# Kernel tuning notes

Measured on AMD Instinct MI355X. Metric: run time of the kernel, lower is better.

The kernel has to match this reference:

```python
import jax, jax.numpy as jnp
import numpy as np

EPS = 1e-6
NQ, NKV, D, HID = 40, 8, 128, 5120
QKV_DIM = (NQ + 2 * NKV) * D + NQ  # gating enabled


def rmsnorm(x, w):
    xf = x.astype(jnp.float32)
    n = jax.lax.rsqrt(jnp.mean(xf * xf, axis=-1, keepdims=True) + EPS)
    return (xf * n).astype(x.dtype) * w


def rope(x, cos, sin):
    # x: [B,S,h,d], cos/sin: [B,S,d]
    d = x.shape[-1]
    c = cos[..., None, :d]
    s = sin[..., None, :d]
    x1, x2 = x[..., : d // 2], x[..., d // 2 :]
    rot = jnp.concatenate([-x2, x1], axis=-1)
    return x * c + rot * s


def setup_inputs() -> dict:
    key = jax.random.key(0)
    ks = jax.random.split(key, 8)
    B, S = 1, 2048
    return {
        "x": jax.random.normal(ks[0], (B, S, HID), jnp.float32),
        "rope_cos": jax.random.normal(ks[1], (B, S, D), jnp.float32),
        "rope_sin": jax.random.normal(ks[2], (B, S, D), jnp.float32),
        "w_pre_norm": jnp.ones((HID,), jnp.float32),
        "w_qkv": jax.random.normal(ks[3], (HID, QKV_DIM), jnp.float32) * 0.02,
        "w_q_norm": jnp.ones((D,), jnp.float32),
        "w_k_norm": jnp.ones((D,), jnp.float32),
        "w_proj": jax.random.normal(ks[4], (NQ * D, HID), jnp.float32) * 0.02,
    }


def reference(x, rope_cos, rope_sin, w_pre_norm, w_qkv, w_q_norm, w_k_norm, w_proj):
    B, S, _ = x.shape
    normed = rmsnorm(x, w_pre_norm)
    qkv = normed @ w_qkv  # [B,S,QKV_DIM]
    q_dim, k_dim = NQ * D, NKV * D
    q = qkv[..., :q_dim].reshape(B, S, NQ, D)
    k = qkv[..., q_dim : q_dim + k_dim].reshape(B, S, NKV, D)
    v = qkv[..., q_dim + k_dim : q_dim + 2 * k_dim].reshape(B, S, NKV, D)
    gate = jax.nn.sigmoid(qkv[..., q_dim + 2 * k_dim :])  # [B,S,NQ]
    q = rmsnorm(q, w_q_norm)
    k = rmsnorm(k, w_k_norm)
    q = rope(q, rope_cos, rope_sin)
    k = rope(k, rope_cos, rope_sin)
    # GQA: expand kv groups to query heads
    rep = NQ // NKV
    k = jnp.repeat(k, rep, axis=2)  # [B,S,NQ,D]
    v = jnp.repeat(v, rep, axis=2)
    scale = 1.0 / jnp.sqrt(jnp.float32(D))
    scores = jnp.einsum("bqhd,bkhd->bhqk", q, k) * scale
    attn = jax.nn.softmax(scores, axis=-1)
    out = jnp.einsum("bhqk,bkhd->bqhd", attn, v)  # [B,S,NQ,D]
    out = out * gate[..., None]
    out = out.reshape(B, S, NQ * D)
    return out @ w_proj
```

## Files before the change

### kernel.cpp

```cpp
#include <hip/hip_runtime.h>
#include <hip/hip_bf16.h>
#include <stdint.h>

#define S_LEN 2048
#define NQh   40
#define NKVh  8
#define HD    128
#define HIDd  5120
#define QKV_C 7208
#define QKV_P 7424
#define NROW  (S_LEN * NQh)

typedef unsigned short u16;
typedef short bf16x8 __attribute__((ext_vector_type(8)));
typedef float f32x4  __attribute__((ext_vector_type(4)));
typedef u16   u16x4  __attribute__((ext_vector_type(4)));

typedef const __attribute__((address_space(1))) void* gas_ptr;
typedef __attribute__((address_space(3))) void*       las_ptr;

#define MFMA16(a, b, c) __builtin_amdgcn_mfma_f32_16x16x32_bf16(a, b, c, 0, 0, 0)

__device__ __forceinline__ u16 f2bf(float f) {
  union { float f; unsigned u; } v; v.f = f;
  return (u16)((v.u + 0x7fffu + ((v.u >> 16) & 1u)) >> 16);
}
__device__ __forceinline__ u16 f2bf_c(float f) {
  union { __hip_bfloat16 b; u16 u; } v;
  v.b = __float2bfloat16(f);
  return v.u;
}
__device__ __forceinline__ float b2f(u16 b) {
  union { unsigned u; float f; } v; v.u = ((unsigned)b) << 16; return v.f;
}

__device__ __forceinline__ float wave_sum64(float x) {
#pragma unroll
  for (int m = 32; m > 0; m >>= 1) x += __shfl_xor(x, m, 64);
  return x;
}

__global__ __launch_bounds__(256) void prenorm_kernel(
    const float* __restrict__ x, const float* __restrict__ w, u16* __restrict__ xn) {
  int row = blockIdx.x;
  const float4* xr = (const float4*)(x + (size_t)row * HIDd);
  const float4* wr = (const float4*)w;
  float4 vx[5];
  float ss = 0.f;
#pragma unroll
  for (int c = 0; c < 5; ++c) {
    int i = c * 256 + threadIdx.x;
    vx[c] = xr[i];
    ss += vx[c].x * vx[c].x + vx[c].y * vx[c].y + vx[c].z * vx[c].z + vx[c].w * vx[c].w;
  }
  ss = wave_sum64(ss);
  __shared__ float red[4];
  if ((threadIdx.x & 63) == 0) red[threadIdx.x >> 6] = ss;
  __syncthreads();
  float tot = red[0] + red[1] + red[2] + red[3];
  float n = rsqrtf(tot * (1.f / HIDd) + 1e-6f);
  u16x4* out = (u16x4*)(xn + (size_t)row * HIDd);
#pragma unroll
  for (int c = 0; c < 5; ++c) {
    int i = c * 256 + threadIdx.x;
    float4 vw = wr[i];
    u16x4 o;
    o.x = f2bf(vx[c].x * n * vw.x);
    o.y = f2bf(vx[c].y * n * vw.y);
    o.z = f2bf(vx[c].z * n * vw.z);
    o.w = f2bf(vx[c].w * n * vw.w);
    out[i] = o;
  }
}

__global__ __launch_bounds__(256) void transpose_cvt(
    const float* __restrict__ src, u16* __restrict__ dst,
    int C, long ld_src, long ld_dst, long srcZ, long dstZ) {
  src += (long)blockIdx.z * srcZ;
  dst += (long)blockIdx.z * dstZ;
  __shared__ float t[32][34];
  int c0 = blockIdx.x * 32, r0 = blockIdx.y * 32;
  {
    int lc = threadIdx.x & 15, lr = threadIdx.x >> 4;
#pragma unroll
    for (int i = 0; i < 32; i += 16) {
      int r = r0 + lr + i;
      int c = c0 + lc * 2;
      float2 v = make_float2(0.f, 0.f);
      if (c < C) v = *(const float2*)(src + (long)r * ld_src + c);
      *(float2*)&t[lr + i][lc * 2] = v;
    }
  }
  __syncthreads();
  {
    int cc = threadIdx.x >> 3;
    int rq = (threadIdx.x & 7) * 4;
    int c = c0 + cc;
    if (c < C) {
      u16x4 o;
#pragma unroll
      for (int rr = 0; rr < 4; ++rr) o[rr] = f2bf(t[rq + rr][cc]);
      *(u16x4*)(dst + (long)c * ld_dst + (r0 + rq)) = o;
    }
  }
}

__global__ __launch_bounds__(512, 1) void gemm8(
    const u16* __restrict__ A, const u16* __restrict__ BT, float* __restrict__ C,
    int M, int N, int K) {
  __shared__ __align__(16) char AL[65536];
  __shared__ __align__(16) char BL[65536];

  int tid = threadIdx.x, w = tid >> 6, l = tid & 63;
  int wm = w >> 2, wn = w & 3;
  int g = l >> 4, q = l & 15;

  int nwg = gridDim.x * gridDim.y;
  int wgid = blockIdx.y * gridDim.x + blockIdx.x;
  int cpx = nwg >> 3;
  int swz = (wgid & 7) * cpx + (wgid >> 3);
  int bx = swz % gridDim.x, by = swz / gridDim.x;
  long mBase = (long)by * 256, nBase = (long)bx * 256;
  long Kb = (long)K * 2;
  const char* Ag = (const char*)A + mBase * Kb;
  const char* Bg = (const char*)BT + nBase * Kb;

  int d0 = tid * 16, d1 = 8192 + tid * 16;
  long soff0 = (long)(d0 >> 6) * Kb + ((d0 & 63) ^ (((d0 >> 7) & 3) << 4));
  long soff1 = (long)(d1 >> 6) * Kb + ((d1 & 63) ^ (((d1 >> 7) & 3) << 4));

#define STG1(GBASE, LDSB, BUF, KH, T_)                                          \
  do {                                                                          \
    long kb_ = (long)(T_) * 128 + (KH) * 64;                                    \
    __builtin_amdgcn_global_load_lds((gas_ptr)((GBASE) + soff0 + kb_),          \
        (las_ptr)((LDSB) + (BUF) * 32768 + (KH) * 16384 + d0), 16, 0, 0);       \
    __builtin_amdgcn_global_load_lds((gas_ptr)((GBASE) + soff1 + kb_),          \
        (las_ptr)((LDSB) + (BUF) * 32768 + (KH) * 16384 + d1), 16, 0, 0);       \
  } while (0)

#define BARR                                                                    \
  do {                                                                          \
    __builtin_amdgcn_s_barrier();                                               \
    __builtin_amdgcn_sched_barrier(0);                                          \
  } while (0)
#define VMW(NLIT)                                                               \
  do {                                                                          \
    asm volatile("s_waitcnt vmcnt(" #NLIT ")" ::: "memory");                    \
    __builtin_amdgcn_sched_barrier(0);                                          \
  } while (0)

  int offA[8], offB[4];
#pragma unroll
  for (int i = 0; i < 8; ++i) {
    int r = wm * 128 + i * 16 + q;
    offA[i] = r * 64 + ((g * 16) ^ (((r >> 1) & 3) << 4));
  }
#pragma unroll
  for (int j = 0; j < 4; ++j) {
    int r = wn * 64 + j * 16 + q;
    offB[j] = r * 64 + ((g * 16) ^ (((r >> 1) & 3) << 4));
  }

#define RD_ALL(ABASE, BBASE)                                                    \
  do {                                                                          \
    _Pragma("unroll") for (int ii = 0; ii < 8; ++ii)                            \
      af[ii] = *(const bf16x8*)((ABASE) + offA[ii]);                            \
    _Pragma("unroll") for (int j = 0; j < 4; ++j)                               \
      bfr[j] = *(const bf16x8*)((BBASE) + offB[j]);                             \
  } while (0)
#define MFMA32                                                                  \
  do {                                                                          \
    __builtin_amdgcn_s_setprio(1);                                              \
    _Pragma("unroll") for (int ii = 0; ii < 8; ++ii)                            \
      _Pragma("unroll") for (int j = 0; j < 4; ++j)                             \
        acc[ii][j] = MFMA16(af[ii], bfr[j], acc[ii][j]);                        \
    __builtin_amdgcn_s_setprio(0);                                              \
  } while (0)

  f32x4 acc[8][4] = {};
  int NT = K >> 6;

  STG1(Ag, AL, 0, 0, 0); STG1(Bg, BL, 0, 0, 0);
  STG1(Ag, AL, 0, 1, 0); STG1(Bg, BL, 0, 1, 0);
  STG1(Ag, AL, 1, 0, 1); STG1(Bg, BL, 1, 0, 1);
  VMW(8); BARR;

  for (int t = 0; t < NT; ++t) {
    int buf = t & 1, nb = buf ^ 1;
    const char* Abuf = AL + buf * 32768;
    const char* Bbuf = BL + buf * 32768;
    bf16x8 af[8], bfr[4];

    RD_ALL(Abuf, Bbuf);
    if (t + 1 < NT) { STG1(Ag, AL, nb, 1, t + 1); STG1(Bg, BL, nb, 1, t + 1); VMW(8); }
    else            { VMW(0); }
    BARR;
    MFMA32;
    BARR;

    RD_ALL(Abuf + 16384, Bbuf + 16384);
    if (t + 2 < NT)      { STG1(Ag, AL, buf, 0, t + 2); STG1(Bg, BL, buf, 0, t + 2); VMW(8); }
    else if (t + 1 < NT) { VMW(4); }
    BARR;
    MFMA32;
    BARR;
  }
#undef STG1
#undef RD_ALL
#undef MFMA32
#undef BARR
#undef VMW

#pragma unroll
  for (int i = 0; i < 8; ++i)
#pragma unroll
    for (int j = 0; j < 4; ++j) {
      long mrow = mBase + wm * 128 + i * 16 + g * 4;
      long ncol = nBase + wn * 64 + j * 16 + q;
      float* cp = C + mrow * N + ncol;
#pragma unroll
      for (int r = 0; r < 4; ++r) cp[(long)r * N] = acc[i][j][r];
    }
}

__global__ __launch_bounds__(256) void split_kernel(
    const float* __restrict__ qkv, const float* __restrict__ cosb,
    const float* __restrict__ sinb, const float* __restrict__ wq,
    const float* __restrict__ wk, u16* __restrict__ qb, u16* __restrict__ kb,
    float* __restrict__ gate) {
  int s = blockIdx.x;
  int w = threadIdx.x >> 6, l = threadIdx.x & 63;
  const float* row = qkv + (size_t)s * QKV_P;
  float c0 = cosb[s * HD + l],      s0 = sinb[s * HD + l];
  float c1 = cosb[s * HD + 64 + l], s1 = sinb[s * HD + 64 + l];
  const float SCALE = 0.12751743f;
  for (int h = w; h < NQh; h += 4) {
    float x0 = row[h * HD + l], x1 = row[h * HD + 64 + l];
    float ss = wave_sum64(x0 * x0 + x1 * x1);
    float n = rsqrtf(ss * (1.f / HD) + 1e-6f);
    x0 *= n * wq[l]; x1 *= n * wq[64 + l];
    qb[((size_t)s * NQh + h) * HD + l]      = f2bf((x0 * c0 - x1 * s0) * SCALE);
    qb[((size_t)s * NQh + h) * HD + 64 + l] = f2bf((x1 * c1 + x0 * s1) * SCALE);
  }
  for (int h = w; h < NKVh; h += 4) {
    float x0 = row[NQh * HD + h * HD + l], x1 = row[NQh * HD + h * HD + 64 + l];
    float ss = wave_sum64(x0 * x0 + x1 * x1);
    float n = rsqrtf(ss * (1.f / HD) + 1e-6f);
    x0 *= n * wk[l]; x1 *= n * wk[64 + l];
    kb[((size_t)h * S_LEN + s) * HD + l]      = f2bf(x0 * c0 - x1 * s0);
    kb[((size_t)h * S_LEN + s) * HD + 64 + l] = f2bf(x1 * c1 + x0 * s1);
  }
  if (threadIdx.x < NQh) {
    float gx = row[(NQh + 2 * NKVh) * HD + threadIdx.x];
    gate[(size_t)s * NQh + threadIdx.x] = 1.f / (1.f + expf(-gx));
  }
}

__global__ __launch_bounds__(256) void attn_kernel(
    const u16* __restrict__ qb, const u16* __restrict__ kb,
    const u16* __restrict__ vT,
    u16* __restrict__ opart, float* __restrict__ lpart) {
  int L = blockIdx.x;
  int xcd = L & 7, t0 = L >> 3;
  int G = xcd * 10 + (t0 >> 4);
  int bx = t0 & 15;
  int h = G % NQh, z = G / NQh;
  int hk = h / 5;
  int w = threadIdx.x >> 6, l = threadIdx.x & 63;
  int g = l >> 4, q = l & 15;
  int s0 = bx * 128 + w * 32;
  int tid = threadIdx.x;

  __shared__ __align__(16) u16 Ks[2][32 * 128];
  __shared__ __align__(16) u16 Vs[2][128 * 32];
  __shared__ __align__(16) u16 Plds[4][2][16][40];

  bf16x8 ones;
#pragma unroll
  for (int j = 0; j < 8; ++j) ones[j] = (short)0x3F80;

  bf16x8 qf[2][4];
#pragma unroll
  for (int p = 0; p < 2; ++p)
#pragma unroll
    for (int kk = 0; kk < 4; ++kk)
      qf[p][kk] = *(const bf16x8*)(qb + ((size_t)(s0 + p * 16 + q) * NQh + h) * HD + kk * 32 + g * 8);

  const char* KhB = (const char*)(kb + ((size_t)hk * S_LEN + z * 1024) * HD);
  const char* VhB = (const char*)(vT + (size_t)hk * HD * S_LEN + z * 1024);

  int Dk0 = tid * 16, Dk1 = 4096 + tid * 16;
  long ks0 = (long)(Dk0 >> 8) * 256 + ((Dk0 & 255) ^ (((Dk0 >> 8) & 7) << 4));
  long ks1 = (long)(Dk1 >> 8) * 256 + ((Dk1 & 255) ^ (((Dk1 >> 8) & 7) << 4));
  long vs0 = (long)(Dk0 >> 6) * 4096 + ((Dk0 & 63) ^ (((Dk0 >> 7) & 3) << 4));
  long vs1 = (long)(Dk1 >> 6) * 4096 + ((Dk1 & 63) ^ (((Dk1 >> 7) & 3) << 4));

#define STG(BUF, T_)                                                            \
  do {                                                                          \
    __builtin_amdgcn_global_load_lds((gas_ptr)(KhB + (long)(T_) * 8192 + ks0),  \
        (las_ptr)((char*)&Ks[BUF][0] + Dk0), 16, 0, 0);                         \
    __builtin_amdgcn_global_load_lds((gas_ptr)(KhB + (long)(T_) * 8192 + ks1),  \
        (las_ptr)((char*)&Ks[BUF][0] + Dk1), 16, 0, 0);                         \
    __builtin_amdgcn_global_load_lds((gas_ptr)(VhB + (long)(T_) * 64 + vs0),    \
        (las_ptr)((char*)&Vs[BUF][0] + Dk0), 16, 0, 0);                         \
    __builtin_amdgcn_global_load_lds((gas_ptr)(VhB + (long)(T_) * 64 + vs1),    \
        (las_ptr)((char*)&Vs[BUF][0] + Dk1), 16, 0, 0);                         \
  } while (0)

#define BARR                                                                    \
  do {                                                                          \
    __builtin_amdgcn_sched_barrier(0);                                          \
    __builtin_amdgcn_s_barrier();                                               \
    __builtin_amdgcn_sched_barrier(0);                                          \
  } while (0)

  f32x4 oacc[8][2] = {};
  f32x4 lacc[2] = {};
  int xq = (q & 7) << 4;
  int xv = ((q >> 1) & 3) << 4;

  STG(0, 0); STG(1, 1);
  __builtin_amdgcn_sched_barrier(0);
  asm volatile("s_waitcnt vmcnt(4)" ::: "memory");
  BARR;

  for (int step = 0; step < 32; ++step) {
    const char* kc = (const char*)&Ks[step & 1][0];
    const char* vc = (const char*)&Vs[step & 1][0];

    f32x4 sacc[2][2] = {};
#pragma unroll
    for (int kk = 0; kk < 4; ++kk) {
#pragma unroll
      for (int kt = 0; kt < 2; ++kt) {
        bf16x8 kf = *(const bf16x8*)(kc + (kt * 16 + q) * 256 + ((kk * 64 + g * 16) ^ xq));
        sacc[kt][0] = MFMA16(kf, qf[0][kk], sacc[kt][0]);
        sacc[kt][1] = MFMA16(kf, qf[1][kk], sacc[kt][1]);
      }
    }
    bf16x8 va[8];
#pragma unroll
    for (int dt = 0; dt < 8; ++dt)
      va[dt] = *(const bf16x8*)(vc + (dt * 16 + q) * 64 + ((g * 16) ^ xv));

#pragma unroll
    for (int p = 0; p < 2; ++p) {
#pragma unroll
      for (int kt = 0; kt < 2; ++kt) {
        u16x4 pk;
#pragma unroll
        for (int r = 0; r < 4; ++r) pk[r] = f2bf_c(exp2f(sacc[kt][p][r]));
        *(u16x4*)&Plds[w][p][q][kt * 16 + g * 4] = pk;
      }
    }
    bf16x8 pf0 = *(const bf16x8*)&Plds[w][0][q][g * 8];
    bf16x8 pf1 = *(const bf16x8*)&Plds[w][1][q][g * 8];
    __builtin_amdgcn_s_setprio(1);
#pragma unroll
    for (int dt = 0; dt < 8; ++dt) {
      oacc[dt][0] = MFMA16(va[dt], pf0, oacc[dt][0]);
      oacc[dt][1] = MFMA16(va[dt], pf1, oacc[dt][1]);
    }
    lacc[0] = MFMA16(ones, pf0, lacc[0]);
    lacc[1] = MFMA16(ones, pf1, lacc[1]);
    __builtin_amdgcn_s_setprio(0);

    BARR;
    if (step + 2 < 32) {
      STG(step & 1, step + 2);
      __builtin_amdgcn_sched_barrier(0);
      asm volatile("s_waitcnt vmcnt(4)" ::: "memory");
      __builtin_amdgcn_sched_barrier(0);
    } else if (step + 1 < 32) {
      __builtin_amdgcn_sched_barrier(0);
      asm volatile("s_waitcnt vmcnt(0)" ::: "memory");
      __builtin_amdgcn_sched_barrier(0);
    }
    BARR;
  }
#undef STG
#undef BARR

#pragma unroll
  for (int p = 0; p < 2; ++p) {
    size_t row = (size_t)(s0 + p * 16 + q) * NQh + h;
    if (g == 0) lpart[(size_t)z * NROW + row] = lacc[p][0];
    u16* op = opart + ((size_t)z * NROW + row) * HD;
#pragma unroll
    for (int dt = 0; dt < 8; ++dt) {
      u16x4 o;
#pragma unroll
      for (int r = 0; r < 4; ++r) o[r] = f2bf_c(oacc[dt][p][r]);
      *(u16x4*)(op + dt * 16 + g * 4) = o;
    }
  }
}

__global__ __launch_bounds__(256) void combine_kernel(
    const u16* __restrict__ opart, const float* __restrict__ lpart,
    const float* __restrict__ gate, u16* __restrict__ ob) {
  int t = blockIdx.x * 256 + threadIdx.x;
  int row = t >> 5, dv = (t & 31) * 4;
  float l0 = lpart[row], l1 = lpart[NROW + row];
  float sc = gate[row] / (l0 + l1);
  u16x4 o0 = *(const u16x4*)(opart + (size_t)row * HD + dv);
  u16x4 o1 = *(const u16x4*)(opart + (size_t)NROW * HD + (size_t)row * HD + dv);
  u16x4 o;
#pragma unroll
  for (int r = 0; r < 4; ++r) o[r] = f2bf(sc * (b2f(o0[r]) + b2f(o1[r])));
  *(u16x4*)(ob + (size_t)row * HD + dv) = o;
}

extern "C" void kernel_launch(void* const* d_in, const int* in_sizes, int n_in,
                              void* d_out, int out_size, void* d_ws, size_t ws_size,
                              hipStream_t stream) {
  const float* x     = (const float*)d_in[0];
  const float* rc    = (const float*)d_in[1];
  const float* rs    = (const float*)d_in[2];
  const float* wpre  = (const float*)d_in[3];
  const float* wqkv  = (const float*)d_in[4];
  const float* wqn   = (const float*)d_in[5];
  const float* wkn   = (const float*)d_in[6];
  const float* wproj = (const float*)d_in[7];
  float* out = (float*)d_out;

  char* ws = (char*)d_ws;
  size_t off = 0;
  auto alloc = [&](size_t bytes) -> void* {
    void* p = ws + off;
    off += (bytes + 255) & ~(size_t)255;
    return p;
  };
  u16*   xn     = (u16*)  alloc((size_t)S_LEN * HIDd * 2);
  u16*   wqkvT  = (u16*)  alloc((size_t)QKV_P * HIDd * 2);
  u16*   wprojT = (u16*)  alloc((size_t)HIDd * HIDd * 2);
  float* qkv    = (float*)alloc((size_t)S_LEN * QKV_P * 4);
  u16*   qb     = (u16*)  alloc((size_t)S_LEN * NQh * HD * 2);
  u16*   kb     = (u16*)  alloc((size_t)NKVh * S_LEN * HD * 2);
  u16*   vT     = (u16*)  alloc((size_t)NKVh * HD * S_LEN * 2);
  float* gate   = (float*)alloc((size_t)S_LEN * NQh * 4);
  u16*   ob     = (u16*)  alloc((size_t)S_LEN * NQh * HD * 2);
  if (off > ws_size) return;

  u16*   opart = (u16*)ws;
  float* lpart = (float*)(opart + (size_t)2 * NROW * HD);

  prenorm_kernel<<<S_LEN, 256, 0, stream>>>(x, wpre, xn);
  transpose_cvt<<<dim3(QKV_P / 32, HIDd / 32, 1), 256, 0, stream>>>(
      wqkv, wqkvT, QKV_C, (long)QKV_C, (long)HIDd, 0, 0);
  transpose_cvt<<<dim3(HIDd / 32, HIDd / 32, 1), 256, 0, stream>>>(
      wproj, wprojT, HIDd, (long)HIDd, (long)HIDd, 0, 0);
  gemm8<<<dim3(QKV_P / 256, S_LEN / 256), 512, 0, stream>>>(
      xn, wqkvT, qkv, S_LEN, QKV_P, HIDd);
  split_kernel<<<S_LEN, 256, 0, stream>>>(qkv, rc, rs, wqn, wkn, qb, kb, gate);
  transpose_cvt<<<dim3(HD / 32, S_LEN / 32, NKVh), 256, 0, stream>>>(
      qkv + (NQh + NKVh) * HD, vT, HD, (long)QKV_P, (long)S_LEN,
      128, (long)HD * S_LEN);
  attn_kernel<<<1280, 256, 0, stream>>>(qb, kb, vT, opart, lpart);
  combine_kernel<<<NROW * 32 / 256, 256, 0, stream>>>(
      opart, lpart, gate, ob);
  gemm8<<<dim3(HIDd / 256, S_LEN / 256), 512, 0, stream>>>(
      ob, wprojT, out, S_LEN, HIDd, HIDd);
}
```

Baseline: 622.7 us.

## Store QKV GEMM output as bf16 and use 256x128 tiles for output projection

The QKV projection GEMM now writes bf16 instead of fp32. This halves its write traffic and the reads in split_kernel, and the V transpose becomes a plain bf16 transpose. The gemm8 kernel is templated on N-tile width and output type, and the output projection uses BN=128, which doubles its workgroup count from 160 to 320 so the GPU's compute units are better filled. The cost is extra rounding of Q/K/V/gate to bf16 before normalization, and lower B reuse per tile in the projection.

```diff
diff --git a/kernel.cpp b/kernel.cpp
--- a/kernel.cpp
+++ b/kernel.cpp
@@ -38,6 +38,15 @@
 #pragma unroll
   for (int m = 32; m > 0; m >>= 1) x += __shfl_xor(x, m, 64);
   return x;
+}
+
+__device__ __forceinline__ void cstore(float* cp, long strideN, const f32x4& v) {
+#pragma unroll
+  for (int r = 0; r < 4; ++r) cp[(long)r * strideN] = v[r];
+}
+__device__ __forceinline__ void cstore(u16* cp, long strideN, const f32x4& v) {
+#pragma unroll
+  for (int r = 0; r < 4; ++r) cp[(long)r * strideN] = f2bf_c(v[r]);
 }
 
 __global__ __launch_bounds__(256) void prenorm_kernel(
@@ -105,11 +114,39 @@
   }
 }
 
+__global__ __launch_bounds__(256) void transpose_bf16(
+    const u16* __restrict__ src, u16* __restrict__ dst,
+    long ld_src, long ld_dst, long srcZ, long dstZ) {
+  src += (long)blockIdx.z * srcZ;
+  dst += (long)blockIdx.z * dstZ;
+  __shared__ u16 t[32][34];
+  int c0 = blockIdx.x * 32, r0 = blockIdx.y * 32;
+  {
+    int lc = threadIdx.x & 15, lr = threadIdx.x >> 4;
+#pragma unroll
+    for (int i = 0; i < 32; i += 16)
+      *(unsigned*)&t[lr + i][lc * 2] =
+          *(const unsigned*)(src + (long)(r0 + lr + i) * ld_src + c0 + lc * 2);
+  }
+  __syncthreads();
+  {
+    int cc = threadIdx.x >> 3;
+    int rq = (threadIdx.x & 7) * 4;
+    u16x4 o;
+#pragma unroll
+    for (int rr = 0; rr < 4; ++rr) o[rr] = t[rq + rr][cc];
+    *(u16x4*)(dst + (long)(c0 + cc) * ld_dst + (r0 + rq)) = o;
+  }
+}
+
+template<int BN, typename OutT>
 __global__ __launch_bounds__(512, 1) void gemm8(
-    const u16* __restrict__ A, const u16* __restrict__ BT, float* __restrict__ C,
+    const u16* __restrict__ A, const u16* __restrict__ BT, OutT* __restrict__ C,
     int M, int N, int K) {
+  constexpr int NJ = BN / 64;
+  constexpr int BHALF = BN * 64;
   __shared__ __align__(16) char AL[65536];
-  __shared__ __align__(16) char BL[65536];
+  __shared__ __align__(16) char BL[4 * BHALF];
 
   int tid = threadIdx.x, w = tid >> 6, l = tid & 63;
   int wm = w >> 2, wn = w & 3;
@@ -120,7 +157,7 @@
   int cpx = nwg >> 3;
   int swz = (wgid & 7) * cpx + (wgid >> 3);
   int bx = swz % gridDim.x, by = swz / gridDim.x;
-  long mBase = (long)by * 256, nBase = (long)bx * 256;
+  long mBase = (long)by * 256, nBase = (long)bx * BN;
   long Kb = (long)K * 2;
   const char* Ag = (const char*)A + mBase * Kb;
   const char* Bg = (const char*)BT + nBase * Kb;
@@ -129,13 +166,22 @@
   long soff0 = (long)(d0 >> 6) * Kb + ((d0 & 63) ^ (((d0 >> 7) & 3) << 4));
   long soff1 = (long)(d1 >> 6) * Kb + ((d1 & 63) ^ (((d1 >> 7) & 3) << 4));
 
-#define STG1(GBASE, LDSB, BUF, KH, T_)                                          \
+#define STGA(BUF, KH, T_)                                                       \
   do {                                                                          \
     long kb_ = (long)(T_) * 128 + (KH) * 64;                                    \
-    __builtin_amdgcn_global_load_lds((gas_ptr)((GBASE) + soff0 + kb_),          \
-        (las_ptr)((LDSB) + (BUF) * 32768 + (KH) * 16384 + d0), 16, 0, 0);       \
-    __builtin_amdgcn_global_load_lds((gas_ptr)((GBASE) + soff1 + kb_),          \
-        (las_ptr)((LDSB) + (BUF) * 32768 + (KH) * 16384 + d1), 16, 0, 0);       \
+    __builtin_amdgcn_global_load_lds((gas_ptr)(Ag + soff0 + kb_),               \
+        (las_ptr)(AL + (BUF) * 32768 + (KH) * 16384 + d0), 16, 0, 0);           \
+    __builtin_amdgcn_global_load_lds((gas_ptr)(Ag + soff1 + kb_),               \
+        (las_ptr)(AL + (BUF) * 32768 + (KH) * 16384 + d1), 16, 0, 0);           \
+  } while (0)
+#define STGB(BUF, KH, T_)                                                       \
+  do {                                                                          \
+    long kb_ = (long)(T_) * 128 + (KH) * 64;                                    \
+    __builtin_amdgcn_global_load_lds((gas_ptr)(Bg + soff0 + kb_),               \
+        (las_ptr)(BL + (BUF) * 2 * BHALF + (KH) * BHALF + d0), 16, 0, 0);       \
+    if constexpr (BN == 256)                                                    \
+      __builtin_amdgcn_global_load_lds((gas_ptr)(Bg + soff1 + kb_),             \
+          (las_ptr)(BL + (BUF) * 2 * BHALF + (KH) * BHALF + d1), 16, 0, 0);     \
   } while (0)
 
 #define BARR                                                                    \
@@ -143,21 +189,33 @@
     __builtin_amdgcn_s_barrier();                                               \
     __builtin_amdgcn_sched_barrier(0);                                          \
   } while (0)
-#define VMW(NLIT)                                                               \
-  do {                                                                          \
-    asm volatile("s_waitcnt vmcnt(" #NLIT ")" ::: "memory");                    \
+#define VMW2                                                                    \
+  do {                                                                          \
+    if constexpr (BN == 256) asm volatile("s_waitcnt vmcnt(8)" ::: "memory");   \
+    else                     asm volatile("s_waitcnt vmcnt(6)" ::: "memory");   \
     __builtin_amdgcn_sched_barrier(0);                                          \
   } while (0)
-
-  int offA[8], offB[4];
+#define VMW1                                                                    \
+  do {                                                                          \
+    if constexpr (BN == 256) asm volatile("s_waitcnt vmcnt(4)" ::: "memory");   \
+    else                     asm volatile("s_waitcnt vmcnt(3)" ::: "memory");   \
+    __builtin_amdgcn_sched_barrier(0);                                          \
+  } while (0)
+#define VMW0                                                                    \
+  do {                                                                          \
+    asm volatile("s_waitcnt vmcnt(0)" ::: "memory");                            \
+    __builtin_amdgcn_sched_barrier(0);                                          \
+  } while (0)
+
+  int offA[8], offB[NJ];
 #pragma unroll
   for (int i = 0; i < 8; ++i) {
     int r = wm * 128 + i * 16 + q;
     offA[i] = r * 64 + ((g * 16) ^ (((r >> 1) & 3) << 4));
   }
 #pragma unroll
-  for (int j = 0; j < 4; ++j) {
-    int r = wn * 64 + j * 16 + q;
+  for (int j = 0; j < NJ; ++j) {
+    int r = wn * (BN / 4) + j * 16 + q;
     offB[j] = r * 64 + ((g * 16) ^ (((r >> 1) & 3) << 4));
   }
 
@@ -165,77 +223,78 @@
   do {                                                                          \
     _Pragma("unroll") for (int ii = 0; ii < 8; ++ii)                            \
       af[ii] = *(const bf16x8*)((ABASE) + offA[ii]);                            \
-    _Pragma("unroll") for (int j = 0; j < 4; ++j)                               \
+    _Pragma("unroll") for (int j = 0; j < NJ; ++j)                              \
       bfr[j] = *(const bf16x8*)((BBASE) + offB[j]);                             \
   } while (0)
-#define MFMA32                                                                  \
+#define MFMA_ALL                                                                \
   do {                                                                          \
     __builtin_amdgcn_s_setprio(1);                                              \
     _Pragma("unroll") for (int ii = 0; ii < 8; ++ii)                            \
-      _Pragma("unroll") for (int j = 0; j < 4; ++j)                             \
+      _Pragma("unroll") for (int j = 0; j < NJ; ++j)                            \
         acc[ii][j] = MFMA16(af[ii], bfr[j], acc[ii][j]);                        \
     __builtin_amdgcn_s_setprio(0);                                              \
   } while (0)
 
-  f32x4 acc[8][4] = {};
+  f32x4 acc[8][NJ] = {};
   int NT = K >> 6;
 
-  STG1(Ag, AL, 0, 0, 0); STG1(Bg, BL, 0, 0, 0);
-  STG1(Ag, AL, 0, 1, 0); STG1(Bg, BL, 0, 1, 0);
-  STG1(Ag, AL, 1, 0, 1); STG1(Bg, BL, 1, 0, 1);
-  VMW(8); BARR;
+  STGA(0, 0, 0); STGB(0, 0, 0);
+  STGA(0, 1, 0); STGB(0, 1, 0);
+  STGA(1, 0, 1); STGB(1, 0, 1);
+  VMW2; BARR;
 
   for (int t = 0; t < NT; ++t) {
     int buf = t & 1, nb = buf ^ 1;
     const char* Abuf = AL + buf * 32768;
-    const char* Bbuf = BL + buf * 32768;
-    bf16x8 af[8], bfr[4];
+    const char* Bbuf = BL + buf * 2 * BHALF;
+    bf16x8 af[8], bfr[NJ];
 
     RD_ALL(Abuf, Bbuf);
-    if (t + 1 < NT) { STG1(Ag, AL, nb, 1, t + 1); STG1(Bg, BL, nb, 1, t + 1); VMW(8); }
-    else            { VMW(0); }
+    if (t + 1 < NT) { STGA(nb, 1, t + 1); STGB(nb, 1, t + 1); VMW2; }
+    else            { VMW0; }
     BARR;
-    MFMA32;
+    MFMA_ALL;
     BARR;
 
-    RD_ALL(Abuf + 16384, Bbuf + 16384);
-    if (t + 2 < NT)      { STG1(Ag, AL, buf, 0, t + 2); STG1(Bg, BL, buf, 0, t + 2); VMW(8); }
-    else if (t + 1 < NT) { VMW(4); }
+    RD_ALL(Abuf + 16384, Bbuf + BHALF);
+    if (t + 2 < NT)      { STGA(buf, 0, t + 2); STGB(buf, 0, t + 2); VMW2; }
+    else if (t + 1 < NT) { VMW1; }
     BARR;
-    MFMA32;
+    MFMA_ALL;
     BARR;
   }
-#undef STG1
+#undef STGA
+#undef STGB
 #undef RD_ALL
-#undef MFMA32
+#undef MFMA_ALL
 #undef BARR
-#undef VMW
+#undef VMW2
+#undef VMW1
+#undef VMW0
 
 #pragma unroll
   for (int i = 0; i < 8; ++i)
 #pragma unroll
-    for (int j = 0; j < 4; ++j) {
+    for (int j = 0; j < NJ; ++j) {
       long mrow = mBase + wm * 128 + i * 16 + g * 4;
-      long ncol = nBase + wn * 64 + j * 16 + q;
-      float* cp = C + mrow * N + ncol;
-#pragma unroll
-      for (int r = 0; r < 4; ++r) cp[(long)r * N] = acc[i][j][r];
+      long ncol = nBase + wn * (BN / 4) + j * 16 + q;
+      cstore(C + mrow * N + ncol, N, acc[i][j]);
     }
 }
 
 __global__ __launch_bounds__(256) void split_kernel(
-    const float* __restrict__ qkv, const float* __restrict__ cosb,
+    const u16* __restrict__ qkv, const float* __restrict__ cosb,
     const float* __restrict__ sinb, const float* __restrict__ wq,
     const float* __restrict__ wk, u16* __restrict__ qb, u16* __restrict__ kb,
     float* __restrict__ gate) {
   int s = blockIdx.x;
   int w = threadIdx.x >> 6, l = threadIdx.x & 63;
-  const float* row = qkv + (size_t)s * QKV_P;
+  const u16* row = qkv + (size_t)s * QKV_P;
   float c0 = cosb[s * HD + l],      s0 = sinb[s * HD + l];
   float c1 = cosb[s * HD + 64 + l], s1 = sinb[s * HD + 64 + l];
   const float SCALE = 0.12751743f;
   for (int h = w; h < NQh; h += 4) {
-    float x0 = row[h * HD + l], x1 = row[h * HD + 64 + l];
+    float x0 = b2f(row[h * HD + l]), x1 = b2f(row[h * HD + 64 + l]);
     float ss = wave_sum64(x0 * x0 + x1 * x1);
     float n = rsqrtf(ss * (1.f / HD) + 1e-6f);
     x0 *= n * wq[l]; x1 *= n * wq[64 + l];
@@ -243,7 +302,7 @@
     qb[((size_t)s * NQh + h) * HD + 64 + l] = f2bf((x1 * c1 + x0 * s1) * SCALE);
   }
   for (int h = w; h < NKVh; h += 4) {
-    float x0 = row[NQh * HD + h * HD + l], x1 = row[NQh * HD + h * HD + 64 + l];
+    float x0 = b2f(row[NQh * HD + h * HD + l]), x1 = b2f(row[NQh * HD + h * HD + 64 + l]);
     float ss = wave_sum64(x0 * x0 + x1 * x1);
     float n = rsqrtf(ss * (1.f / HD) + 1e-6f);
     x0 *= n * wk[l]; x1 *= n * wk[64 + l];
@@ -251,7 +310,7 @@
     kb[((size_t)h * S_LEN + s) * HD + 64 + l] = f2bf(x1 * c1 + x0 * s1);
   }
   if (threadIdx.x < NQh) {
-    float gx = row[(NQh + 2 * NKVh) * HD + threadIdx.x];
+    float gx = b2f(row[(NQh + 2 * NKVh) * HD + threadIdx.x]);
     gate[(size_t)s * NQh + threadIdx.x] = 1.f / (1.f + expf(-gx));
   }
 }
@@ -434,7 +493,7 @@
   u16*   xn     = (u16*)  alloc((size_t)S_LEN * HIDd * 2);
   u16*   wqkvT  = (u16*)  alloc((size_t)QKV_P * HIDd * 2);
   u16*   wprojT = (u16*)  alloc((size_t)HIDd * HIDd * 2);
-  float* qkv    = (float*)alloc((size_t)S_LEN * QKV_P * 4);
+  u16*   qkvb   = (u16*)  alloc((size_t)S_LEN * QKV_P * 2);
   u16*   qb     = (u16*)  alloc((size_t)S_LEN * NQh * HD * 2);
   u16*   kb     = (u16*)  alloc((size_t)NKVh * S_LEN * HD * 2);
   u16*   vT     = (u16*)  alloc((size_t)NKVh * HD * S_LEN * 2);
@@ -450,15 +509,15 @@
       wqkv, wqkvT, QKV_C, (long)QKV_C, (long)HIDd, 0, 0);
   transpose_cvt<<<dim3(HIDd / 32, HIDd / 32, 1), 256, 0, stream>>>(
       wproj, wprojT, HIDd, (long)HIDd, (long)HIDd, 0, 0);
-  gemm8<<<dim3(QKV_P / 256, S_LEN / 256), 512, 0, stream>>>(
-      xn, wqkvT, qkv, S_LEN, QKV_P, HIDd);
-  split_kernel<<<S_LEN, 256, 0, stream>>>(qkv, rc, rs, wqn, wkn, qb, kb, gate);
-  transpose_cvt<<<dim3(HD / 32, S_LEN / 32, NKVh), 256, 0, stream>>>(
-      qkv + (NQh + NKVh) * HD, vT, HD, (long)QKV_P, (long)S_LEN,
+  gemm8<256, u16><<<dim3(QKV_P / 256, S_LEN / 256), 512, 0, stream>>>(
+      xn, wqkvT, qkvb, S_LEN, QKV_P, HIDd);
+  split_kernel<<<S_LEN, 256, 0, stream>>>(qkvb, rc, rs, wqn, wkn, qb, kb, gate);
+  transpose_bf16<<<dim3(HD / 32, S_LEN / 32, NKVh), 256, 0, stream>>>(
+      qkvb + (NQh + NKVh) * HD, vT, (long)QKV_P, (long)S_LEN,
       128, (long)HD * S_LEN);
   attn_kernel<<<1280, 256, 0, stream>>>(qb, kb, vT, opart, lpart);
   combine_kernel<<<NROW * 32 / 256, 256, 0, stream>>>(
       opart, lpart, gate, ob);
-  gemm8<<<dim3(HIDd / 256, S_LEN / 256), 512, 0, stream>>>(
+  gemm8<128, float><<<dim3(HIDd / 128, S_LEN / 256), 512, 0, stream>>>(
       ob, wprojT, out, S_LEN, HIDd, HIDd);
 }
```

After: 667.7 us. +7.2%, slower.

## Emit bf16 QKV from GEMM and overlap global prefetch with MFMAs

Applied to the files above, without the earlier changes.

The QKV GEMM now writes bf16 instead of fp32, which halves the intermediate's write and read traffic. The split kernel and the V transpose read bf16 directly, with a new bf16-to-bf16 transpose kernel. The GEMM main loop also issues MFMAs before waiting on global-to-LDS loads and drops one barrier per half-step, so loads and compute overlap more. The risks are extra rounding of QKV before the RMS norm and a possible LDS hazard if the barrier removal races with the next stage's writes.

```diff
diff --git a/kernel.cpp b/kernel.cpp
--- a/kernel.cpp
+++ b/kernel.cpp
@@ -38,6 +38,15 @@
 #pragma unroll
   for (int m = 32; m > 0; m >>= 1) x += __shfl_xor(x, m, 64);
   return x;
+}
+
+__device__ __forceinline__ void cstore(float* cp, long strideN, const f32x4& v) {
+#pragma unroll
+  for (int r = 0; r < 4; ++r) cp[(long)r * strideN] = v[r];
+}
+__device__ __forceinline__ void cstore(u16* cp, long strideN, const f32x4& v) {
+#pragma unroll
+  for (int r = 0; r < 4; ++r) cp[(long)r * strideN] = f2bf_c(v[r]);
 }
 
 __global__ __launch_bounds__(256) void prenorm_kernel(
@@ -105,8 +114,34 @@
   }
 }
 
+__global__ __launch_bounds__(256) void transpose_bf16(
+    const u16* __restrict__ src, u16* __restrict__ dst,
+    long ld_src, long ld_dst, long srcZ, long dstZ) {
+  src += (long)blockIdx.z * srcZ;
+  dst += (long)blockIdx.z * dstZ;
+  __shared__ u16 t[32][34];
+  int c0 = blockIdx.x * 32, r0 = blockIdx.y * 32;
+  {
+    int lc = threadIdx.x & 15, lr = threadIdx.x >> 4;
+#pragma unroll
+    for (int i = 0; i < 32; i += 16)
+      *(unsigned*)&t[lr + i][lc * 2] =
+          *(const unsigned*)(src + (long)(r0 + lr + i) * ld_src + c0 + lc * 2);
+  }
+  __syncthreads();
+  {
+    int cc = threadIdx.x >> 3;
+    int rq = (threadIdx.x & 7) * 4;
+    u16x4 o;
+#pragma unroll
+    for (int rr = 0; rr < 4; ++rr) o[rr] = t[rq + rr][cc];
+    *(u16x4*)(dst + (long)(c0 + cc) * ld_dst + (r0 + rq)) = o;
+  }
+}
+
+template<typename OutT>
 __global__ __launch_bounds__(512, 1) void gemm8(
-    const u16* __restrict__ A, const u16* __restrict__ BT, float* __restrict__ C,
+    const u16* __restrict__ A, const u16* __restrict__ BT, OutT* __restrict__ C,
     int M, int N, int K) {
   __shared__ __align__(16) char AL[65536];
   __shared__ __align__(16) char BL[65536];
@@ -168,7 +203,7 @@
     _Pragma("unroll") for (int j = 0; j < 4; ++j)                               \
       bfr[j] = *(const bf16x8*)((BBASE) + offB[j]);                             \
   } while (0)
-#define MFMA32                                                                  \
+#define MFMA_ALL                                                                \
   do {                                                                          \
     __builtin_amdgcn_s_setprio(1);                                              \
     _Pragma("unroll") for (int ii = 0; ii < 8; ++ii)                            \
@@ -192,22 +227,21 @@
     bf16x8 af[8], bfr[4];
 
     RD_ALL(Abuf, Bbuf);
-    if (t + 1 < NT) { STG1(Ag, AL, nb, 1, t + 1); STG1(Bg, BL, nb, 1, t + 1); VMW(8); }
-    else            { VMW(0); }
+    if (t + 1 < NT) { STG1(Ag, AL, nb, 1, t + 1); STG1(Bg, BL, nb, 1, t + 1); }
+    MFMA_ALL;
+    if (t + 1 < NT) { VMW(8); } else { VMW(0); }
     BARR;
-    MFMA32;
-    BARR;
 
     RD_ALL(Abuf + 16384, Bbuf + 16384);
-    if (t + 2 < NT)      { STG1(Ag, AL, buf, 0, t + 2); STG1(Bg, BL, buf, 0, t + 2); VMW(8); }
+    if (t + 2 < NT) { STG1(Ag, AL, buf, 0, t + 2); STG1(Bg, BL, buf, 0, t + 2); }
+    MFMA_ALL;
+    if (t + 2 < NT)      { VMW(8); }
     else if (t + 1 < NT) { VMW(4); }
     BARR;
-    MFMA32;
-    BARR;
   }
 #undef STG1
 #undef RD_ALL
-#undef MFMA32
+#undef MFMA_ALL
 #undef BARR
 #undef VMW
 
@@ -217,25 +251,23 @@
     for (int j = 0; j < 4; ++j) {
       long mrow = mBase + wm * 128 + i * 16 + g * 4;
       long ncol = nBase + wn * 64 + j * 16 + q;
-      float* cp = C + mrow * N + ncol;
-#pragma unroll
-      for (int r = 0; r < 4; ++r) cp[(long)r * N] = acc[i][j][r];
+      cstore(C + mrow * N + ncol, N, acc[i][j]);
     }
 }
 
 __global__ __launch_bounds__(256) void split_kernel(
-    const float* __restrict__ qkv, const float* __restrict__ cosb,
+    const u16* __restrict__ qkv, const float* __restrict__ cosb,
     const float* __restrict__ sinb, const float* __restrict__ wq,
     const float* __restrict__ wk, u16* __restrict__ qb, u16* __restrict__ kb,
     float* __restrict__ gate) {
   int s = blockIdx.x;
   int w = threadIdx.x >> 6, l = threadIdx.x & 63;
-  const float* row = qkv + (size_t)s * QKV_P;
+  const u16* row = qkv + (size_t)s * QKV_P;
   float c0 = cosb[s * HD + l],      s0 = sinb[s * HD + l];
   float c1 = cosb[s * HD + 64 + l], s1 = sinb[s * HD + 64 + l];
   const float SCALE = 0.12751743f;
   for (int h = w; h < NQh; h += 4) {
-    float x0 = row[h * HD + l], x1 = row[h * HD + 64 + l];
+    float x0 = b2f(row[h * HD + l]), x1 = b2f(row[h * HD + 64 + l]);
     float ss = wave_sum64(x0 * x0 + x1 * x1);
     float n = rsqrtf(ss * (1.f / HD) + 1e-6f);
     x0 *= n * wq[l]; x1 *= n * wq[64 + l];
@@ -243,7 +275,7 @@
     qb[((size_t)s * NQh + h) * HD + 64 + l] = f2bf((x1 * c1 + x0 * s1) * SCALE);
   }
   for (int h = w; h < NKVh; h += 4) {
-    float x0 = row[NQh * HD + h * HD + l], x1 = row[NQh * HD + h * HD + 64 + l];
+    float x0 = b2f(row[NQh * HD + h * HD + l]), x1 = b2f(row[NQh * HD + h * HD + 64 + l]);
     float ss = wave_sum64(x0 * x0 + x1 * x1);
     float n = rsqrtf(ss * (1.f / HD) + 1e-6f);
     x0 *= n * wk[l]; x1 *= n * wk[64 + l];
@@ -251,7 +283,7 @@
     kb[((size_t)h * S_LEN + s) * HD + 64 + l] = f2bf(x1 * c1 + x0 * s1);
   }
   if (threadIdx.x < NQh) {
-    float gx = row[(NQh + 2 * NKVh) * HD + threadIdx.x];
+    float gx = b2f(row[(NQh + 2 * NKVh) * HD + threadIdx.x]);
     gate[(size_t)s * NQh + threadIdx.x] = 1.f / (1.f + expf(-gx));
   }
 }
@@ -434,7 +466,7 @@
   u16*   xn     = (u16*)  alloc((size_t)S_LEN * HIDd * 2);
   u16*   wqkvT  = (u16*)  alloc((size_t)QKV_P * HIDd * 2);
   u16*   wprojT = (u16*)  alloc((size_t)HIDd * HIDd * 2);
-  float* qkv    = (float*)alloc((size_t)S_LEN * QKV_P * 4);
+  u16*   qkvb   = (u16*)  alloc((size_t)S_LEN * QKV_P * 2);
   u16*   qb     = (u16*)  alloc((size_t)S_LEN * NQh * HD * 2);
   u16*   kb     = (u16*)  alloc((size_t)NKVh * S_LEN * HD * 2);
   u16*   vT     = (u16*)  alloc((size_t)NKVh * HD * S_LEN * 2);
@@ -450,15 +482,15 @@
       wqkv, wqkvT, QKV_C, (long)QKV_C, (long)HIDd, 0, 0);
   transpose_cvt<<<dim3(HIDd / 32, HIDd / 32, 1), 256, 0, stream>>>(
       wproj, wprojT, HIDd, (long)HIDd, (long)HIDd, 0, 0);
-  gemm8<<<dim3(QKV_P / 256, S_LEN / 256), 512, 0, stream>>>(
-      xn, wqkvT, qkv, S_LEN, QKV_P, HIDd);
-  split_kernel<<<S_LEN, 256, 0, stream>>>(qkv, rc, rs, wqn, wkn, qb, kb, gate);
-  transpose_cvt<<<dim3(HD / 32, S_LEN / 32, NKVh), 256, 0, stream>>>(
-      qkv + (NQh + NKVh) * HD, vT, HD, (long)QKV_P, (long)S_LEN,
+  gemm8<u16><<<dim3(QKV_P / 256, S_LEN / 256), 512, 0, stream>>>(
+      xn, wqkvT, qkvb, S_LEN, QKV_P, HIDd);
+  split_kernel<<<S_LEN, 256, 0, stream>>>(qkvb, rc, rs, wqn, wkn, qb, kb, gate);
+  transpose_bf16<<<dim3(HD / 32, S_LEN / 32, NKVh), 256, 0, stream>>>(
+      qkvb + (NQh + NKVh) * HD, vT, (long)QKV_P, (long)S_LEN,
       128, (long)HD * S_LEN);
   attn_kernel<<<1280, 256, 0, stream>>>(qb, kb, vT, opart, lpart);
   combine_kernel<<<NROW * 32 / 256, 256, 0, stream>>>(
       opart, lpart, gate, ob);
-  gemm8<<<dim3(HIDd / 256, S_LEN / 256), 512, 0, stream>>>(
+  gemm8<float><<<dim3(HIDd / 256, S_LEN / 256), 512, 0, stream>>>(
       ob, wprojT, out, S_LEN, HIDd, HIDd);
 }
```

Result: faster. 571.8 us (-8.2%).
